# Kernel tuning notes

Measured on AMD Instinct MI355X. Metric: run time of the kernel, lower is better.

Reference implementation:

```python
import jax, jax.numpy as jnp
import numpy as np

BN_EPS = 1e-5

# Octonion multiplication table: hamilton block (r, c) = SIGN[c][r] * a[IDX[c][r]]
IDX = np.array([
    [0,1,2,3,4,5,6,7],
    [1,0,3,2,5,4,7,6],
    [2,3,0,1,6,7,4,5],
    [3,2,1,0,7,6,5,4],
    [4,5,6,7,0,1,2,3],
    [5,4,7,6,1,0,3,2],
    [6,7,4,5,2,3,0,1],
    [7,6,5,4,3,2,1,0]], dtype=np.int32)
SIGN = np.array([
    [ 1, 1, 1, 1, 1, 1, 1, 1],
    [ 1,-1, 1,-1, 1,-1,-1, 1],
    [ 1,-1,-1, 1, 1, 1,-1,-1],
    [ 1, 1,-1,-1, 1,-1, 1,-1],
    [ 1,-1,-1,-1,-1, 1, 1, 1],
    [ 1, 1,-1, 1,-1,-1,-1, 1],
    [ 1, 1, 1,-1,-1, 1,-1,-1],
    [ 1,-1, 1, 1,-1,-1, 1,-1]], dtype=np.float32)

def make_octonion_mul(kernel):
    # kernel: [in/8, out]; split cols into 8 chunks a0..a7 of [in/8, out/8]
    in8, out = kernel.shape
    out8 = out // 8
    a = kernel.reshape(in8, 8, out8).transpose(1, 0, 2)  # [8, in/8, out/8]
    blocks = jnp.asarray(SIGN)[:, :, None, None] * a[jnp.asarray(IDX)]  # [c, r, in/8, out/8]
    # hamilton[r*in8:(r+1)*in8, c*out8:(c+1)*out8] = blocks[c, r]
    return jnp.transpose(blocks, (1, 2, 0, 3)).reshape(8 * in8, out)  # [in, out]

def setup_inputs() -> dict:
    key = jax.random.key(0)
    ks = jax.random.split(key, 5)
    N, E, D_IN, D_OUT = 100000, 3200000, 256, 256
    stdv = float(np.sqrt(6.0 / (D_IN // 8 + D_OUT)))
    return {
        "x": jax.random.normal(ks[0], (N, D_IN), dtype=jnp.float32),
        "weight": jax.random.uniform(ks[1], (D_IN // 8, D_OUT), dtype=jnp.float32,
                                      minval=-stdv, maxval=stdv),
        "gamma": jnp.ones((D_OUT,), dtype=jnp.float32),
        "beta": jnp.zeros((D_OUT,), dtype=jnp.float32),
        "edge_weight": jax.random.uniform(ks[2], (E,), dtype=jnp.float32),
        "edge_src": jax.random.randint(ks[3], (E,), 0, N, dtype=jnp.int32),
        "edge_dst": jax.random.randint(ks[4], (E,), 0, N, dtype=jnp.int32),
    }

def reference(x, weight, gamma, beta, edge_weight, edge_src, edge_dst):
    N = x.shape[0]
    hamilton = make_octonion_mul(weight)          # [in, out]
    support = x @ hamilton                        # [N, out]
    # sparse adjacency aggregation: out[dst] += w * support[src]
    msgs = edge_weight[:, None] * support[edge_src]
    out = jax.ops.segment_sum(msgs, edge_dst, num_segments=N)  # [N, out]
    # BatchNorm1d (training mode: batch stats, biased variance)
    mean = jnp.mean(out, axis=0)
    var = jnp.var(out, axis=0)
    out = (out - mean) * jax.lax.rsqrt(var + BN_EPS) * gamma + beta
    return jnp.tanh(out)
```

## Files before the change

### kernel.cpp

```cpp
#include <hip/hip_runtime.h>
#include <cmath>

#define NB 512
#define CAP 7168
#define CHUNK 8192

typedef short short8 __attribute__((ext_vector_type(8)));
typedef float f32x4 __attribute__((ext_vector_type(4)));

__constant__ int c_IDX[64] = {
  0,1,2,3,4,5,6,7,
  1,0,3,2,5,4,7,6,
  2,3,0,1,6,7,4,5,
  3,2,1,0,7,6,5,4,
  4,5,6,7,0,1,2,3,
  5,4,7,6,1,0,3,2,
  6,7,4,5,2,3,0,1,
  7,6,5,4,3,2,1,0};
__constant__ float c_SIGN[64] = {
  1,1,1,1,1,1,1,1,
  1,-1,1,-1,1,-1,-1,1,
  1,-1,-1,1,1,1,-1,-1,
  1,1,-1,-1,1,-1,1,-1,
  1,-1,-1,-1,-1,1,1,1,
  1,1,-1,1,-1,-1,-1,1,
  1,1,1,-1,-1,1,-1,-1,
  1,-1,1,1,-1,-1,1,-1};

__device__ inline unsigned bf16_rne(float f) {
  unsigned u = __float_as_uint(f);
  return (u + 0x7fffu + ((u >> 16) & 1u)) >> 16;
}
__device__ inline unsigned bfpack(float lo, float hi) {
  return bf16_rne(lo) | (bf16_rne(hi) << 16);
}

__global__ __launch_bounds__(256) void prep_kernel(const float* __restrict__ weight,
                                                   unsigned short* __restrict__ hi,
                                                   unsigned short* __restrict__ lo,
                                                   int* __restrict__ binCursor,
                                                   float* __restrict__ bnsum,
                                                   const float4* __restrict__ x4,
                                                   uint2* __restrict__ xh, size_t n4) {
  const int tid = threadIdx.x;
  if (blockIdx.x == 0) {
    #pragma unroll
    for (int k = 0; k < NB / 256; k++) binCursor[k * 256 + tid] = 0;
    bnsum[tid] = 0.f;
    bnsum[256 + tid] = 0.f;
  }
  if (blockIdx.x < 256) {
    int idx = blockIdx.x * 256 + tid;
    int col = idx >> 8, k = idx & 255;
    int r = k >> 5, i = k & 31, c = col >> 5, o = col & 31;
    float v = c_SIGN[c * 8 + r] * weight[i * 256 + c_IDX[c * 8 + r] * 32 + o];
    unsigned hb = bf16_rne(v);
    float hf = __uint_as_float(hb << 16);
    hi[idx] = (unsigned short)hb;
    lo[idx] = (unsigned short)bf16_rne(v - hf);
  }
  size_t idx = (size_t)blockIdx.x * 256 + tid;
  size_t stride = (size_t)gridDim.x * 256;
  for (size_t i = idx; i < n4; i += stride) {
    float4 v = x4[i];
    xh[i] = make_uint2(bfpack(v.x, v.y), bfpack(v.z, v.w));
  }
}

__global__ __launch_bounds__(256) void bin_scatter(const int* __restrict__ src,
                                                   const int* __restrict__ dst,
                                                   const float* __restrict__ w,
                                                   int* __restrict__ binCursor,
                                                   int2* __restrict__ bb, int E, int N) {
  __shared__ int hist[NB];
  __shared__ int lcur[NB];
  int tid = threadIdx.x;
  int base = blockIdx.x * CHUNK;
  int end = base + CHUNK; if (end > E) end = E;
  for (int i = tid; i < NB; i += 256) hist[i] = 0;
  __syncthreads();
  for (int i = base + tid; i < end; i += 256)
    atomicAdd(&hist[(int)((long long)dst[i] * NB / N)], 1);
  __syncthreads();
  for (int i = tid; i < NB; i += 256) {
    int h = hist[i];
    lcur[i] = h ? atomicAdd(&binCursor[i], h) : 0;
  }
  __syncthreads();
  for (int i = base + tid; i < end; i += 256) {
    int d = dst[i];
    int b = (int)((long long)d * NB / N);
    int d0 = (int)(((long long)b * N + NB - 1) / NB);
    int pos = atomicAdd(&lcur[b], 1);
    if (pos < CAP)
      bb[(size_t)b * CAP + pos] = make_int2(src[i] | ((d - d0) << 24), __float_as_int(w[i]));
  }
}

__global__ __launch_bounds__(256) void bin_place(const int2* __restrict__ bb,
                                                 const int* __restrict__ binCursor,
                                                 int* __restrict__ off,
                                                 int* __restrict__ cnt,
                                                 int2* __restrict__ edges, int N) {
  __shared__ int lcnt[208];
  __shared__ int loff[208];
  int b = blockIdx.x, tid = threadIdx.x;
  int d0 = (int)(((long long)b * N + NB - 1) / NB);
  int d1 = (int)(((long long)(b + 1) * N + NB - 1) / NB);
  if (d1 > N) d1 = N;
  int nd = d1 - d0;
  int tot = binCursor[b]; if (tot > CAP) tot = CAP;
  const size_t sb = (size_t)b * CAP;
  for (int i = tid; i < nd; i += 256) lcnt[i] = 0;
  __syncthreads();
  for (int i = tid; i < tot; i += 256)
    atomicAdd(&lcnt[((unsigned)bb[sb + i].x) >> 24], 1);
  __syncthreads();
  if (tid == 0) {
    int s = 0;
    for (int i = 0; i < nd; i++) { loff[i] = s; s += lcnt[i]; }
  }
  __syncthreads();
  for (int i = tid; i < nd; i += 256) {
    off[d0 + i] = (int)sb + loff[i];
    cnt[d0 + i] = lcnt[i];
  }
  __syncthreads();
  for (int i = tid; i < nd; i += 256) lcnt[i] = loff[i];
  __syncthreads();
  for (int i = tid; i < tot; i += 256) {
    int2 e = bb[sb + i];
    int pos = atomicAdd(&lcnt[((unsigned)e.x) >> 24], 1);
    edges[sb + pos] = make_int2(e.x & 0xFFFFFF, e.y);
  }
}

__device__ inline void acc4(float& a0, float& a1, float& a2, float& a3,
                            uint2 v, float w) {
  a0 = fmaf(w, __uint_as_float(v.x << 16), a0);
  a1 = fmaf(w, __uint_as_float(v.x & 0xffff0000u), a1);
  a2 = fmaf(w, __uint_as_float(v.y << 16), a2);
  a3 = fmaf(w, __uint_as_float(v.y & 0xffff0000u), a3);
}

__global__ __launch_bounds__(256) void gather_kernel(const uint2* __restrict__ x8,
                                                     const int2* __restrict__ edges,
                                                     const int* __restrict__ off,
                                                     const int* __restrict__ cnt,
                                                     uint2* __restrict__ agg8, int N) {
  int d = blockIdx.x * 4 + (threadIdx.x >> 6);
  if (d >= N) return;
  int c = threadIdx.x & 63;
  int start = off[d], n = cnt[d];
  float a0 = 0.f, a1 = 0.f, a2 = 0.f, a3 = 0.f;
  int t = 0;
  for (; t + 8 <= n; t += 8) {
    int2 e0 = edges[start + t + 0];
    int2 e1 = edges[start + t + 1];
    int2 e2 = edges[start + t + 2];
    int2 e3 = edges[start + t + 3];
    int2 e4 = edges[start + t + 4];
    int2 e5 = edges[start + t + 5];
    int2 e6 = edges[start + t + 6];
    int2 e7 = edges[start + t + 7];
    uint2 v0 = x8[(size_t)e0.x * 64 + c];
    uint2 v1 = x8[(size_t)e1.x * 64 + c];
    uint2 v2 = x8[(size_t)e2.x * 64 + c];
    uint2 v3 = x8[(size_t)e3.x * 64 + c];
    uint2 v4 = x8[(size_t)e4.x * 64 + c];
    uint2 v5 = x8[(size_t)e5.x * 64 + c];
    uint2 v6 = x8[(size_t)e6.x * 64 + c];
    uint2 v7 = x8[(size_t)e7.x * 64 + c];
    acc4(a0, a1, a2, a3, v0, __int_as_float(e0.y));
    acc4(a0, a1, a2, a3, v1, __int_as_float(e1.y));
    acc4(a0, a1, a2, a3, v2, __int_as_float(e2.y));
    acc4(a0, a1, a2, a3, v3, __int_as_float(e3.y));
    acc4(a0, a1, a2, a3, v4, __int_as_float(e4.y));
    acc4(a0, a1, a2, a3, v5, __int_as_float(e5.y));
    acc4(a0, a1, a2, a3, v6, __int_as_float(e6.y));
    acc4(a0, a1, a2, a3, v7, __int_as_float(e7.y));
  }
  for (; t < n; t++) {
    int2 e0 = edges[start + t];
    uint2 v0 = x8[(size_t)e0.x * 64 + c];
    acc4(a0, a1, a2, a3, v0, __int_as_float(e0.y));
  }
  agg8[(size_t)d * 64 + c] = make_uint2(bfpack(a0, a1), bfpack(a2, a3));
}

__global__ __launch_bounds__(512) void mfma_gemm(const uint4* __restrict__ aggh,
                                                 const unsigned short* __restrict__ hamT_hi,
                                                 const unsigned short* __restrict__ hamT_lo,
                                                 float* __restrict__ bnsum,
                                                 unsigned short* __restrict__ obuf, int N) {
  __shared__ __align__(16) unsigned short Al[128 * 256];
  __shared__ float csum[256], csq[256];
  const int tid = threadIdx.x;
  const int row0 = blockIdx.x * 128;
  const int lane = tid & 63, wv = tid >> 6;
  const int wm = wv >> 2, wn = wv & 3;

  if (tid < 256) { csum[tid] = 0.f; csq[tid] = 0.f; }

  #pragma unroll
  for (int it = 0; it < 8; it++) {
    int cidx = it * 512 + tid;
    int row = cidx >> 5, c16 = cidx & 31;
    int rg = row0 + row;
    uint4 v = make_uint4(0u, 0u, 0u, 0u);
    if (rg < N) v = aggh[(size_t)rg * 32 + c16];
    *(uint4*)((char*)Al + row * 512 + ((c16 * 16) ^ ((row & 7) << 4))) = v;
  }
  __syncthreads();

  f32x4 acc[4][4];
  #pragma unroll
  for (int m = 0; m < 4; m++)
    #pragma unroll
    for (int n = 0; n < 4; n++) acc[m][n] = (f32x4)0.f;

  const char* bh = (const char*)hamT_hi;
  const char* bl = (const char*)hamT_lo;
  #pragma unroll
  for (int kk = 0; kk < 8; kk++) {
    const int kbyte = (lane >> 4) * 16 + kk * 64;
    short8 af[4];
    #pragma unroll
    for (int m = 0; m < 4; m++) {
      int row = wm * 64 + m * 16 + (lane & 15);
      af[m] = *(const short8*)((const char*)Al + row * 512 + (kbyte ^ ((row & 7) << 4)));
    }
    #pragma unroll
    for (int n = 0; n < 4; n++) {
      int colg = wn * 64 + n * 16 + (lane & 15);
      size_t boff = (size_t)colg * 512 + kbyte;
      short8 bhv = *(const short8*)(bh + boff);
      short8 blv = *(const short8*)(bl + boff);
      #pragma unroll
      for (int m = 0; m < 4; m++)
        acc[m][n] = __builtin_amdgcn_mfma_f32_16x16x32_bf16(af[m], bhv, acc[m][n], 0, 0, 0);
      #pragma unroll
      for (int m = 0; m < 4; m++)
        acc[m][n] = __builtin_amdgcn_mfma_f32_16x16x32_bf16(af[m], blv, acc[m][n], 0, 0, 0);
    }
  }

  #pragma unroll
  for (int n = 0; n < 4; n++) {
    int colg = wn * 64 + n * 16 + (lane & 15);
    float s = 0.f, q = 0.f;
    #pragma unroll
    for (int m = 0; m < 4; m++) {
      int rgb = row0 + wm * 64 + m * 16 + (lane >> 4) * 4;
      #pragma unroll
      for (int r = 0; r < 4; r++) {
        float v = acc[m][n][r];
        s += v; q = fmaf(v, v, q);
        int rg = rgb + r;
        if (rg < N) obuf[(size_t)rg * 256 + colg] = (unsigned short)bf16_rne(v);
      }
    }
    s += __shfl_xor(s, 16); s += __shfl_xor(s, 32);
    q += __shfl_xor(q, 16); q += __shfl_xor(q, 32);
    if (lane < 16) {
      atomicAdd(&csum[wn * 64 + n * 16 + lane], s);
      atomicAdd(&csq [wn * 64 + n * 16 + lane], q);
    }
  }
  __syncthreads();
  if (tid < 256) {
    atomicAdd(&bnsum[tid], csum[tid]);
    atomicAdd(&bnsum[256 + tid], csq[tid]);
  }
}

__global__ __launch_bounds__(256) void final_kernel(const uint2* __restrict__ obuf,
                                                    float* __restrict__ out,
                                                    const float* __restrict__ bnsum,
                                                    const float* __restrict__ gamma,
                                                    const float* __restrict__ beta,
                                                    float invN, size_t total4) {
  size_t idx = (size_t)blockIdx.x * 256 + threadIdx.x;
  size_t stride = (size_t)gridDim.x * 256;
  int c0 = (int)((idx * 4) & 255);
  float sc[4], ofs[4];
  #pragma unroll
  for (int j = 0; j < 4; j++) {
    float mean = bnsum[c0 + j] * invN;
    float var  = bnsum[256 + c0 + j] * invN - mean * mean;
    float s = rsqrtf(var + 1e-5f) * gamma[c0 + j];
    sc[j] = s;
    ofs[j] = beta[c0 + j] - mean * s;
  }
  float4* out4 = (float4*)out;
  for (size_t i = idx; i < total4; i += stride) {
    uint2 u = obuf[i];
    float4 v;
    v.x = tanhf(fmaf(__uint_as_float(u.x << 16),         sc[0], ofs[0]));
    v.y = tanhf(fmaf(__uint_as_float(u.x & 0xffff0000u), sc[1], ofs[1]));
    v.z = tanhf(fmaf(__uint_as_float(u.y << 16),         sc[2], ofs[2]));
    v.w = tanhf(fmaf(__uint_as_float(u.y & 0xffff0000u), sc[3], ofs[3]));
    out4[i] = v;
  }
}

extern "C" void kernel_launch(void* const* d_in, const int* in_sizes, int n_in,
                              void* d_out, int out_size, void* d_ws, size_t ws_size,
                              hipStream_t stream) {
  const float* x      = (const float*)d_in[0];
  const float* weight = (const float*)d_in[1];
  const float* gamma  = (const float*)d_in[2];
  const float* beta   = (const float*)d_in[3];
  const float* ew     = (const float*)d_in[4];
  const int*   esrc   = (const int*)d_in[5];
  const int*   edst   = (const int*)d_in[6];
  const int N = in_sizes[0] / 256;
  const int E = in_sizes[4];
  float* out = (float*)d_out;

  char* p = (char*)d_ws;
  auto alloc = [&](size_t bytes) {
    char* q = p;
    p += (bytes + 255) & ~(size_t)255;
    return q;
  };
  unsigned short* hamT_hi = (unsigned short*)alloc(65536 * 2);
  unsigned short* hamT_lo = (unsigned short*)alloc(65536 * 2);
  int*   binCursor = (int*)alloc(NB * 4);
  int*   cnt       = (int*)alloc((size_t)N * 4);
  int*   off       = (int*)alloc((size_t)N * 4);
  int2*  bb        = (int2*)alloc((size_t)NB * CAP * 8);
  int2*  edges     = (int2*)alloc((size_t)NB * CAP * 8);
  uint2* xh        = (uint2*)alloc((size_t)N * 256 * 2);
  uint4* aggh      = (uint4*)alloc((size_t)N * 256 * 2);
  float* bnsum     = (float*)alloc(512 * 4);
  unsigned short* obuf = (unsigned short*)bb;

  const int gridE = (E + CHUNK - 1) / CHUNK;
  const int rowBlocks = (N + 127) / 128;

  prep_kernel<<<2048, 256, 0, stream>>>(weight, hamT_hi, hamT_lo, binCursor, bnsum,
                                        (const float4*)x, xh, (size_t)N * 64);
  bin_scatter<<<gridE, 256, 0, stream>>>(esrc, edst, ew, binCursor, bb, E, N);
  bin_place<<<NB, 256, 0, stream>>>(bb, binCursor, off, cnt, edges, N);
  gather_kernel<<<(N + 3) / 4, 256, 0, stream>>>((const uint2*)xh, edges, off, cnt,
                                                 (uint2*)aggh, N);
  mfma_gemm<<<rowBlocks, 512, 0, stream>>>(aggh, hamT_hi, hamT_lo, bnsum, obuf, N);
  final_kernel<<<2048, 256, 0, stream>>>((const uint2*)obuf, out, bnsum, gamma, beta,
                                         1.f / (float)N, (size_t)N * 64);
}
```

Baseline: 478.0 us.

## Fuse bin placement into gather via shared-memory edge sort per bin

Merges the bin_place and gather kernels into one binGather kernel with one 1024-thread block per destination bin. Each block counting-sorts its bin's edges into LDS, then gathers source rows, so the global edges/off/cnt arrays and their round trip are gone. The x-to-bf16 conversion moves from prep_kernel into bin_scatter, which shrinks prep_kernel to 256 blocks. The risk is that only 512 large blocks with about 57KB of LDS each run the gather, which limits occupancy and load balance compared with the old per-node grid.

```diff
diff --git a/kernel.cpp b/kernel.cpp
--- a/kernel.cpp
+++ b/kernel.cpp
@@ -39,9 +39,7 @@
                                                    unsigned short* __restrict__ hi,
                                                    unsigned short* __restrict__ lo,
                                                    int* __restrict__ binCursor,
-                                                   float* __restrict__ bnsum,
-                                                   const float4* __restrict__ x4,
-                                                   uint2* __restrict__ xh, size_t n4) {
+                                                   float* __restrict__ bnsum) {
   const int tid = threadIdx.x;
   if (blockIdx.x == 0) {
     #pragma unroll
@@ -49,29 +47,23 @@
     bnsum[tid] = 0.f;
     bnsum[256 + tid] = 0.f;
   }
-  if (blockIdx.x < 256) {
-    int idx = blockIdx.x * 256 + tid;
-    int col = idx >> 8, k = idx & 255;
-    int r = k >> 5, i = k & 31, c = col >> 5, o = col & 31;
-    float v = c_SIGN[c * 8 + r] * weight[i * 256 + c_IDX[c * 8 + r] * 32 + o];
-    unsigned hb = bf16_rne(v);
-    float hf = __uint_as_float(hb << 16);
-    hi[idx] = (unsigned short)hb;
-    lo[idx] = (unsigned short)bf16_rne(v - hf);
-  }
-  size_t idx = (size_t)blockIdx.x * 256 + tid;
-  size_t stride = (size_t)gridDim.x * 256;
-  for (size_t i = idx; i < n4; i += stride) {
-    float4 v = x4[i];
-    xh[i] = make_uint2(bfpack(v.x, v.y), bfpack(v.z, v.w));
-  }
+  int idx = blockIdx.x * 256 + tid;
+  int col = idx >> 8, k = idx & 255;
+  int r = k >> 5, i = k & 31, c = col >> 5, o = col & 31;
+  float v = c_SIGN[c * 8 + r] * weight[i * 256 + c_IDX[c * 8 + r] * 32 + o];
+  unsigned hb = bf16_rne(v);
+  float hf = __uint_as_float(hb << 16);
+  hi[idx] = (unsigned short)hb;
+  lo[idx] = (unsigned short)bf16_rne(v - hf);
 }
 
 __global__ __launch_bounds__(256) void bin_scatter(const int* __restrict__ src,
                                                    const int* __restrict__ dst,
                                                    const float* __restrict__ w,
                                                    int* __restrict__ binCursor,
-                                                   int2* __restrict__ bb, int E, int N) {
+                                                   int2* __restrict__ bb, int E, int N,
+                                                   const float4* __restrict__ x4,
+                                                   uint2* __restrict__ xh, size_t n4) {
   __shared__ int hist[NB];
   __shared__ int lcur[NB];
   int tid = threadIdx.x;
@@ -95,43 +87,11 @@
     if (pos < CAP)
       bb[(size_t)b * CAP + pos] = make_int2(src[i] | ((d - d0) << 24), __float_as_int(w[i]));
   }
-}
-
-__global__ __launch_bounds__(256) void bin_place(const int2* __restrict__ bb,
-                                                 const int* __restrict__ binCursor,
-                                                 int* __restrict__ off,
-                                                 int* __restrict__ cnt,
-                                                 int2* __restrict__ edges, int N) {
-  __shared__ int lcnt[208];
-  __shared__ int loff[208];
-  int b = blockIdx.x, tid = threadIdx.x;
-  int d0 = (int)(((long long)b * N + NB - 1) / NB);
-  int d1 = (int)(((long long)(b + 1) * N + NB - 1) / NB);
-  if (d1 > N) d1 = N;
-  int nd = d1 - d0;
-  int tot = binCursor[b]; if (tot > CAP) tot = CAP;
-  const size_t sb = (size_t)b * CAP;
-  for (int i = tid; i < nd; i += 256) lcnt[i] = 0;
-  __syncthreads();
-  for (int i = tid; i < tot; i += 256)
-    atomicAdd(&lcnt[((unsigned)bb[sb + i].x) >> 24], 1);
-  __syncthreads();
-  if (tid == 0) {
-    int s = 0;
-    for (int i = 0; i < nd; i++) { loff[i] = s; s += lcnt[i]; }
-  }
-  __syncthreads();
-  for (int i = tid; i < nd; i += 256) {
-    off[d0 + i] = (int)sb + loff[i];
-    cnt[d0 + i] = lcnt[i];
-  }
-  __syncthreads();
-  for (int i = tid; i < nd; i += 256) lcnt[i] = loff[i];
-  __syncthreads();
-  for (int i = tid; i < tot; i += 256) {
-    int2 e = bb[sb + i];
-    int pos = atomicAdd(&lcnt[((unsigned)e.x) >> 24], 1);
-    edges[sb + pos] = make_int2(e.x & 0xFFFFFF, e.y);
+  size_t idx = (size_t)blockIdx.x * 256 + tid;
+  size_t stride = (size_t)gridDim.x * 256;
+  for (size_t i = idx; i < n4; i += stride) {
+    float4 v = x4[i];
+    xh[i] = make_uint2(bfpack(v.x, v.y), bfpack(v.z, v.w));
   }
 }
 
@@ -143,49 +103,80 @@
   a3 = fmaf(w, __uint_as_float(v.y & 0xffff0000u), a3);
 }
 
-__global__ __launch_bounds__(256) void gather_kernel(const uint2* __restrict__ x8,
-                                                     const int2* __restrict__ edges,
-                                                     const int* __restrict__ off,
-                                                     const int* __restrict__ cnt,
-                                                     uint2* __restrict__ agg8, int N) {
-  int d = blockIdx.x * 4 + (threadIdx.x >> 6);
-  if (d >= N) return;
-  int c = threadIdx.x & 63;
-  int start = off[d], n = cnt[d];
-  float a0 = 0.f, a1 = 0.f, a2 = 0.f, a3 = 0.f;
-  int t = 0;
-  for (; t + 8 <= n; t += 8) {
-    int2 e0 = edges[start + t + 0];
-    int2 e1 = edges[start + t + 1];
-    int2 e2 = edges[start + t + 2];
-    int2 e3 = edges[start + t + 3];
-    int2 e4 = edges[start + t + 4];
-    int2 e5 = edges[start + t + 5];
-    int2 e6 = edges[start + t + 6];
-    int2 e7 = edges[start + t + 7];
-    uint2 v0 = x8[(size_t)e0.x * 64 + c];
-    uint2 v1 = x8[(size_t)e1.x * 64 + c];
-    uint2 v2 = x8[(size_t)e2.x * 64 + c];
-    uint2 v3 = x8[(size_t)e3.x * 64 + c];
-    uint2 v4 = x8[(size_t)e4.x * 64 + c];
-    uint2 v5 = x8[(size_t)e5.x * 64 + c];
-    uint2 v6 = x8[(size_t)e6.x * 64 + c];
-    uint2 v7 = x8[(size_t)e7.x * 64 + c];
-    acc4(a0, a1, a2, a3, v0, __int_as_float(e0.y));
-    acc4(a0, a1, a2, a3, v1, __int_as_float(e1.y));
-    acc4(a0, a1, a2, a3, v2, __int_as_float(e2.y));
-    acc4(a0, a1, a2, a3, v3, __int_as_float(e3.y));
-    acc4(a0, a1, a2, a3, v4, __int_as_float(e4.y));
-    acc4(a0, a1, a2, a3, v5, __int_as_float(e5.y));
-    acc4(a0, a1, a2, a3, v6, __int_as_float(e6.y));
-    acc4(a0, a1, a2, a3, v7, __int_as_float(e7.y));
-  }
-  for (; t < n; t++) {
-    int2 e0 = edges[start + t];
-    uint2 v0 = x8[(size_t)e0.x * 64 + c];
-    acc4(a0, a1, a2, a3, v0, __int_as_float(e0.y));
-  }
-  agg8[(size_t)d * 64 + c] = make_uint2(bfpack(a0, a1), bfpack(a2, a3));
+__global__ __launch_bounds__(1024) void binGather(const uint2* __restrict__ x8,
+                                                  const int2* __restrict__ bb,
+                                                  const int* __restrict__ binCursor,
+                                                  uint2* __restrict__ agg8, int N) {
+  __shared__ int2 eb[CAP];
+  __shared__ int lcnt[208];
+  __shared__ int loff[209];
+  const int b = blockIdx.x, tid = threadIdx.x;
+  const int d0 = (int)(((long long)b * N + NB - 1) / NB);
+  int d1 = (int)(((long long)(b + 1) * N + NB - 1) / NB);
+  if (d1 > N) d1 = N;
+  const int nd = d1 - d0;
+  int tot = binCursor[b]; if (tot > CAP) tot = CAP;
+  const size_t sb = (size_t)b * CAP;
+
+  for (int i = tid; i < nd; i += 1024) lcnt[i] = 0;
+  __syncthreads();
+  for (int i = tid; i < tot; i += 1024)
+    atomicAdd(&lcnt[((unsigned)bb[sb + i].x) >> 24], 1);
+  __syncthreads();
+  if (tid == 0) {
+    int s = 0;
+    for (int i = 0; i < nd; i++) { loff[i] = s; s += lcnt[i]; }
+    loff[nd] = s;
+  }
+  __syncthreads();
+  for (int i = tid; i < nd; i += 1024) lcnt[i] = loff[i];
+  __syncthreads();
+  for (int i = tid; i < tot; i += 1024) {
+    int2 e = bb[sb + i];
+    int pos = atomicAdd(&lcnt[((unsigned)e.x) >> 24], 1);
+    eb[pos] = make_int2(e.x & 0xFFFFFF, e.y);
+  }
+  __syncthreads();
+
+  const int wv = tid >> 6, c = tid & 63;
+  for (int dl = wv; dl < nd; dl += 16) {
+    const int start = loff[dl];
+    const int n = loff[dl + 1] - start;
+    float a0 = 0.f, a1 = 0.f, a2 = 0.f, a3 = 0.f;
+    int t = 0;
+    for (; t + 8 <= n; t += 8) {
+      int2 e0 = eb[start + t + 0];
+      int2 e1 = eb[start + t + 1];
+      int2 e2 = eb[start + t + 2];
+      int2 e3 = eb[start + t + 3];
+      int2 e4 = eb[start + t + 4];
+      int2 e5 = eb[start + t + 5];
+      int2 e6 = eb[start + t + 6];
+      int2 e7 = eb[start + t + 7];
+      uint2 v0 = x8[(size_t)e0.x * 64 + c];
+      uint2 v1 = x8[(size_t)e1.x * 64 + c];
+      uint2 v2 = x8[(size_t)e2.x * 64 + c];
+      uint2 v3 = x8[(size_t)e3.x * 64 + c];
+      uint2 v4 = x8[(size_t)e4.x * 64 + c];
+      uint2 v5 = x8[(size_t)e5.x * 64 + c];
+      uint2 v6 = x8[(size_t)e6.x * 64 + c];
+      uint2 v7 = x8[(size_t)e7.x * 64 + c];
+      acc4(a0, a1, a2, a3, v0, __int_as_float(e0.y));
+      acc4(a0, a1, a2, a3, v1, __int_as_float(e1.y));
+      acc4(a0, a1, a2, a3, v2, __int_as_float(e2.y));
+      acc4(a0, a1, a2, a3, v3, __int_as_float(e3.y));
+      acc4(a0, a1, a2, a3, v4, __int_as_float(e4.y));
+      acc4(a0, a1, a2, a3, v5, __int_as_float(e5.y));
+      acc4(a0, a1, a2, a3, v6, __int_as_float(e6.y));
+      acc4(a0, a1, a2, a3, v7, __int_as_float(e7.y));
+    }
+    for (; t < n; t++) {
+      int2 e0 = eb[start + t];
+      uint2 v0 = x8[(size_t)e0.x * 64 + c];
+      acc4(a0, a1, a2, a3, v0, __int_as_float(e0.y));
+    }
+    agg8[(size_t)(d0 + dl) * 64 + c] = make_uint2(bfpack(a0, a1), bfpack(a2, a3));
+  }
 }
 
 __global__ __launch_bounds__(512) void mfma_gemm(const uint4* __restrict__ aggh,
@@ -327,10 +318,7 @@
   unsigned short* hamT_hi = (unsigned short*)alloc(65536 * 2);
   unsigned short* hamT_lo = (unsigned short*)alloc(65536 * 2);
   int*   binCursor = (int*)alloc(NB * 4);
-  int*   cnt       = (int*)alloc((size_t)N * 4);
-  int*   off       = (int*)alloc((size_t)N * 4);
   int2*  bb        = (int2*)alloc((size_t)NB * CAP * 8);
-  int2*  edges     = (int2*)alloc((size_t)NB * CAP * 8);
   uint2* xh        = (uint2*)alloc((size_t)N * 256 * 2);
   uint4* aggh      = (uint4*)alloc((size_t)N * 256 * 2);
   float* bnsum     = (float*)alloc(512 * 4);
@@ -339,12 +327,11 @@
   const int gridE = (E + CHUNK - 1) / CHUNK;
   const int rowBlocks = (N + 127) / 128;
 
-  prep_kernel<<<2048, 256, 0, stream>>>(weight, hamT_hi, hamT_lo, binCursor, bnsum,
-                                        (const float4*)x, xh, (size_t)N * 64);
-  bin_scatter<<<gridE, 256, 0, stream>>>(esrc, edst, ew, binCursor, bb, E, N);
-  bin_place<<<NB, 256, 0, stream>>>(bb, binCursor, off, cnt, edges, N);
-  gather_kernel<<<(N + 3) / 4, 256, 0, stream>>>((const uint2*)xh, edges, off, cnt,
-                                                 (uint2*)aggh, N);
+  prep_kernel<<<256, 256, 0, stream>>>(weight, hamT_hi, hamT_lo, binCursor, bnsum);
+  bin_scatter<<<gridE, 256, 0, stream>>>(esrc, edst, ew, binCursor, bb, E, N,
+                                         (const float4*)x, xh, (size_t)N * 64);
+  binGather<<<NB, 1024, 0, stream>>>((const uint2*)xh, bb, binCursor,
+                                     (uint2*)aggh, N);
   mfma_gemm<<<rowBlocks, 512, 0, stream>>>(aggh, hamT_hi, hamT_lo, bnsum, obuf, N);
   final_kernel<<<2048, 256, 0, stream>>>((const uint2*)obuf, out, bnsum, gamma, beta,
                                          1.f / (float)N, (size_t)N * 64);
```

New measurement: 474.6 us. No clear change (-0.7%).
